# Performance work log

Measured on AMD Instinct MI355X. Metric: run time of the kernel, lower is better.

The kernel has to match this reference:

```python
import jax, jax.numpy as jnp
import numpy as np

N_MODEL = 1024
N_HEADS = 16
KV_HEADS = 4
HEAD_DIM = N_MODEL // N_HEADS          # 64
KV_MODEL = HEAD_DIM * KV_HEADS         # 256
GROUPS = N_HEADS // KV_HEADS           # 4
B, S = 4, 2048


def _rmsnorm(x):
    return x * jax.lax.rsqrt(jnp.mean(x * x, axis=-1, keepdims=True) + 1e-6)


def _act_quant(x):
    # 8-bit absmax per-token quantization (BitNet b1.58)
    scale = 127.0 / jnp.clip(jnp.max(jnp.abs(x), axis=-1, keepdims=True), 1e-5)
    return jnp.clip(jnp.round(x * scale), -128.0, 127.0) / scale


def _weight_quant(w):
    # ternary absmean quantization
    scale = 1.0 / jnp.clip(jnp.mean(jnp.abs(w)), 1e-5)
    return jnp.clip(jnp.round(w * scale), -1.0, 1.0) / scale


def bitlinear(x, w, b):
    xn = _rmsnorm(x)
    xq = xn + jax.lax.stop_gradient(_act_quant(xn) - xn)   # STE
    wq = w + jax.lax.stop_gradient(_weight_quant(w) - w)   # STE
    return jnp.einsum('...i,oi->...o', xq, wq) + b


def setup_inputs() -> dict:
    key = jax.random.key(0)
    ks = jax.random.split(key, 11)
    sq = 1.0 / np.sqrt(N_MODEL)
    sk = 1.0 / np.sqrt(KV_MODEL)
    return {
        'query': jax.random.normal(ks[0], (B, S, N_MODEL), jnp.float32),
        'key':   jax.random.normal(ks[1], (B, S, N_MODEL), jnp.float32),
        'value': jax.random.normal(ks[2], (B, S, N_MODEL), jnp.float32),
        'Wq': jax.random.normal(ks[3], (N_MODEL, N_MODEL), jnp.float32) * sq,
        'bq': jnp.zeros((N_MODEL,), jnp.float32),
        'Wk': jax.random.normal(ks[4], (KV_MODEL, N_MODEL), jnp.float32) * sq,
        'bk': jnp.zeros((KV_MODEL,), jnp.float32),
        'Wv': jax.random.normal(ks[5], (KV_MODEL, N_MODEL), jnp.float32) * sq,
        'bv': jnp.zeros((KV_MODEL,), jnp.float32),
        'Wo': jax.random.normal(ks[6], (N_MODEL, KV_MODEL), jnp.float32) * sk,
        'bo': jnp.zeros((N_MODEL,), jnp.float32),
    }


def reference(query, key, value, Wq, bq, Wk, bk, Wv, bv, Wo, bo):
    b = query.shape[0]
    Q = bitlinear(query, Wq, bq)   # [b, n, n_model]
    K = bitlinear(key,   Wk, bk)   # [b, s, kv_model]
    V = bitlinear(value, Wv, bv)   # [b, s, kv_model]

    # [b, h, n, d] layouts
    Q = Q.reshape(b, -1, N_HEADS, HEAD_DIM).transpose(0, 2, 1, 3)
    K = K.reshape(b, -1, KV_HEADS, HEAD_DIM).transpose(0, 2, 1, 3)
    V = V.reshape(b, -1, KV_HEADS, HEAD_DIM).transpose(0, 2, 1, 3)

    # group query heads: [b, g, kv_h, n, d]
    Qg = Q.reshape(b, KV_HEADS, GROUPS, -1, HEAD_DIM).transpose(0, 2, 1, 3, 4)
    # NOTE: faithful to the module, the einsum output has no 'g' axis,
    # so the grouped query heads are SUMMED over g.
    energy = jnp.einsum('bghnd,bhsd->bhns', Qg, K)  # [b, kv_h, n, s]

    scale = jnp.sqrt(jnp.float32(HEAD_DIM))
    attention = jax.nn.softmax(energy / scale, axis=-1)
    x = jnp.einsum('bhns,bhsd->bhnd', attention, V)  # [b, kv_h, n, d]
    x = x.transpose(0, 2, 1, 3).reshape(b, -1, KV_MODEL)
    x = bitlinear(x, Wo, bo)       # [b, n, n_model]
    return (x, attention)
```

## Files before the change

### kernel.cpp

```cpp
#include <hip/hip_runtime.h>
#include <stdint.h>

#define N_MODELC 1024
#define KV_MODELC 256
#define BATCH 4
#define SEQ 2048
#define NTOK (BATCH*SEQ)
#define NCHUNK 4
#define CHUNK (SEQ/NCHUNK)

typedef __attribute__((ext_vector_type(4))) float f32x4;
typedef __attribute__((ext_vector_type(4))) int   i32x4;
typedef __attribute__((ext_vector_type(8))) short s16x8;

__device__ __forceinline__ unsigned short f2bf(float f){
  unsigned u = __builtin_bit_cast(unsigned, f);
  u = (u + 0x7FFFu + ((u>>16)&1u)) >> 16;
  return (unsigned short)u;
}

__global__ __launch_bounds__(256) void k_actquant1024(
    const float* __restrict__ xq_in, const float* __restrict__ xk_in, const float* __restrict__ xv_in,
    int8_t* __restrict__ q8q, int8_t* __restrict__ q8k, int8_t* __restrict__ q8v,
    float* __restrict__ scq, float* __restrict__ sck, float* __restrict__ scv)
{
  int row = blockIdx.x, which = blockIdx.y, t = threadIdx.x;
  const float* x = (which==0)?xq_in:(which==1)?xk_in:xv_in;
  int8_t* q8 = (which==0)?q8q:(which==1)?q8k:q8v;
  float* sc = (which==0)?scq:(which==1)?sck:scv;
  const float* xr = x + (size_t)row*N_MODELC;
  float4 v = reinterpret_cast<const float4*>(xr)[t];
  float ss = v.x*v.x + v.y*v.y + v.z*v.z + v.w*v.w;
  float am = fmaxf(fmaxf(fabsf(v.x),fabsf(v.y)), fmaxf(fabsf(v.z),fabsf(v.w)));
  #pragma unroll
  for (int m=32;m;m>>=1){ ss += __shfl_xor(ss,m,64); am = fmaxf(am, __shfl_xor(am,m,64)); }
  __shared__ float red[8];
  int wid = t>>6;
  if ((t&63)==0){ red[wid]=ss; red[4+wid]=am; }
  __syncthreads();
  ss = red[0]+red[1]+red[2]+red[3];
  am = fmaxf(fmaxf(red[4],red[5]), fmaxf(red[6],red[7]));
  float rinv = rsqrtf(ss*(1.0f/N_MODELC) + 1e-6f);
  float clipv = fmaxf(am*rinv, 1e-5f);
  float qs = 127.0f/clipv;
  float fsc = rinv*qs;
  char4 o;
  o.x = (signed char)(int)fminf(127.f, fmaxf(-128.f, rintf(v.x*fsc)));
  o.y = (signed char)(int)fminf(127.f, fmaxf(-128.f, rintf(v.y*fsc)));
  o.z = (signed char)(int)fminf(127.f, fmaxf(-128.f, rintf(v.z*fsc)));
  o.w = (signed char)(int)fminf(127.f, fmaxf(-128.f, rintf(v.w*fsc)));
  reinterpret_cast<char4*>(q8 + (size_t)row*N_MODELC)[t] = o;
  if (t==0) sc[row] = clipv*(1.0f/127.0f);
}

__global__ __launch_bounds__(64) void k_actquant256(
    const float* __restrict__ X, int8_t* __restrict__ q8, float* __restrict__ sc)
{
  int row = blockIdx.x, l = threadIdx.x;
  float4 v = reinterpret_cast<const float4*>(X + (size_t)row*KV_MODELC)[l];
  float ss = v.x*v.x + v.y*v.y + v.z*v.z + v.w*v.w;
  float am = fmaxf(fmaxf(fabsf(v.x),fabsf(v.y)), fmaxf(fabsf(v.z),fabsf(v.w)));
  #pragma unroll
  for (int m=32;m;m>>=1){ ss += __shfl_xor(ss,m,64); am = fmaxf(am, __shfl_xor(am,m,64)); }
  float rinv = rsqrtf(ss*(1.0f/KV_MODELC) + 1e-6f);
  float clipv = fmaxf(am*rinv, 1e-5f);
  float qs = 127.0f/clipv;
  float fsc = rinv*qs;
  char4 o;
  o.x = (signed char)(int)fminf(127.f, fmaxf(-128.f, rintf(v.x*fsc)));
  o.y = (signed char)(int)fminf(127.f, fmaxf(-128.f, rintf(v.y*fsc)));
  o.z = (signed char)(int)fminf(127.f, fmaxf(-128.f, rintf(v.z*fsc)));
  o.w = (signed char)(int)fminf(127.f, fmaxf(-128.f, rintf(v.w*fsc)));
  reinterpret_cast<char4*>(q8 + (size_t)row*KV_MODELC)[l] = o;
  if (l==0) sc[row] = clipv*(1.0f/127.0f);
}

__global__ __launch_bounds__(256) void k_wabs_partial(
    const float* __restrict__ Wq, const float* __restrict__ Wk,
    const float* __restrict__ Wv, const float* __restrict__ Wo, float* __restrict__ partial)
{
  int mat = blockIdx.y;
  const float* w = (mat==0)?Wq:(mat==1)?Wk:(mat==2)?Wv:Wo;
  int n = (mat==0)?(N_MODELC*N_MODELC):(KV_MODELC*N_MODELC);
  float s = 0.f;
  for (int i = blockIdx.x*256 + threadIdx.x; i < n; i += 256*256) s += fabsf(w[i]);
  #pragma unroll
  for (int m=32;m;m>>=1) s += __shfl_xor(s,m,64);
  __shared__ float red[4];
  int wid = threadIdx.x>>6;
  if ((threadIdx.x&63)==0) red[wid]=s;
  __syncthreads();
  if (threadIdx.x==0) partial[mat*256 + blockIdx.x] = red[0]+red[1]+red[2]+red[3];
}

__global__ __launch_bounds__(256) void k_wfinal(const float* __restrict__ partial, float* __restrict__ wfac)
{
  int mat = blockIdx.x, t = threadIdx.x;
  float s = partial[mat*256 + t];
  #pragma unroll
  for (int m=32;m;m>>=1) s += __shfl_xor(s,m,64);
  __shared__ float red[4];
  int wid = t>>6;
  if ((t&63)==0) red[wid]=s;
  __syncthreads();
  if (t==0){
    float tot = red[0]+red[1]+red[2]+red[3];
    float n = (mat==0)?(float)(N_MODELC*N_MODELC):(float)(KV_MODELC*N_MODELC);
    wfac[mat] = fmaxf(tot/n, 1e-5f);
  }
}

__global__ __launch_bounds__(256) void k_tern(
    const float* __restrict__ Wq, const float* __restrict__ Wk,
    const float* __restrict__ Wv, const float* __restrict__ Wo,
    const float* __restrict__ wfac,
    int8_t* __restrict__ Wqs, int8_t* __restrict__ Wkt,
    int8_t* __restrict__ Wvt, int8_t* __restrict__ Wot)
{
  int mat = blockIdx.y;
  int idx = blockIdx.x*256 + threadIdx.x;
  if (mat==0){
    float s = 1.0f/wfac[0];
    int op = idx>>10, i = idx&1023;
    int kv = op>>6, d = op&63;
    int acc = 0;
    #pragma unroll
    for (int g=0; g<4; g++){
      float w = Wq[(size_t)(kv*256 + g*64 + d)*N_MODELC + i];
      float r = fminf(1.f, fmaxf(-1.f, rintf(w*s)));
      acc += (int)r;
    }
    Wqs[idx] = (int8_t)acc;
  } else {
    const float* w = (mat==1)?Wk:(mat==2)?Wv:Wo;
    int8_t* o = (mat==1)?Wkt:(mat==2)?Wvt:Wot;
    float s = 1.0f/wfac[mat];
    float r = fminf(1.f, fmaxf(-1.f, rintf(w[idx]*s)));
    o[idx] = (int8_t)r;
  }
}

template<int KDIM, int MODE>
__global__ __launch_bounds__(256) void k_gemm_i8(
    const int8_t* __restrict__ A, const int8_t* __restrict__ B,
    const float* __restrict__ rowscale, const float* __restrict__ wfac, int wfi,
    const float* __restrict__ bias, void* __restrict__ outp)
{
  int mb = blockIdx.x*64, nb = blockIdx.y*64;
  int w = threadIdx.x>>6, l = threadIdx.x&63, lr = l&15, lk = l>>4;
  const int8_t* Ap = A + (size_t)(mb + w*16 + lr)*KDIM + lk*16;
  const int8_t* Bp = B + (size_t)(nb + lr)*KDIM + lk*16;
  i32x4 acc[4];
  #pragma unroll
  for (int f=0; f<4; f++) acc[f] = i32x4{0,0,0,0};
  #pragma unroll 4
  for (int kk=0; kk<KDIM; kk+=64){
    i32x4 a = *reinterpret_cast<const i32x4*>(Ap + kk);
    #pragma unroll
    for (int f=0; f<4; f++){
      i32x4 b = *reinterpret_cast<const i32x4*>(Bp + (size_t)f*16*KDIM + kk);
      acc[f] = __builtin_amdgcn_mfma_i32_16x16x64_i8(a, b, acc[f], 0, 0, 0);
    }
  }
  float wf = wfac[wfi];
  #pragma unroll
  for (int f=0; f<4; f++){
    int col = nb + f*16 + lr;
    float bval;
    if constexpr (MODE==0){
      int kv = col>>6, d = col&63;
      const float* bb = bias + kv*256 + d;
      bval = bb[0]+bb[64]+bb[128]+bb[192];
    } else {
      bval = bias[col];
    }
    #pragma unroll
    for (int r=0; r<4; r++){
      int row = mb + w*16 + lk*4 + r;
      float val = (float)acc[f][r] * (rowscale[row]*wf) + bval;
      if constexpr (MODE==0){
        ((unsigned short*)outp)[(size_t)row*KV_MODELC + col] = f2bf(0.125f*val);
      } else if constexpr (MODE==1){
        ((unsigned short*)outp)[(size_t)row*KV_MODELC + col] = f2bf(val);
      } else if constexpr (MODE==2){
        int bi = row>>11, s = row&2047;
        ((unsigned short*)outp)[((size_t)(bi*256 + col))*SEQ + s] = f2bf(val);
      } else {
        ((float*)outp)[(size_t)row*N_MODELC + col] = val;
      }
    }
  }
}

__global__ __launch_bounds__(256) void k_attn1(
    const unsigned short* __restrict__ Qs, const unsigned short* __restrict__ Kb,
    float* __restrict__ mpart, float* __restrict__ lpart)
{
  int bkv = blockIdx.y, b = bkv>>2, kv = bkv&3;
  int c = blockIdx.z;
  int w = threadIdx.x>>6, l = threadIdx.x&63, lr = l&15, lk = l>>4;
  int rowt = blockIdx.x*64 + w*16;
  size_t tq = (size_t)(b*SEQ + rowt + lr)*KV_MODELC + kv*64 + lk*8;
  s16x8 qa0 = *reinterpret_cast<const s16x8*>(Qs + tq);
  s16x8 qa1 = *reinterpret_cast<const s16x8*>(Qs + tq + 32);
  const unsigned short* kbase = Kb + (size_t)b*SEQ*KV_MODELC + kv*64 + lk*8;
  float m[4], ll[4];
  #pragma unroll
  for (int r=0;r<4;r++){ m[r] = -INFINITY; ll[r] = 0.f; }
  for (int st=c*CHUNK; st<(c+1)*CHUNK; st+=16){
    const unsigned short* kp = kbase + (size_t)(st+lr)*KV_MODELC;
    s16x8 k0 = *reinterpret_cast<const s16x8*>(kp);
    s16x8 k1 = *reinterpret_cast<const s16x8*>(kp + 32);
    f32x4 acc = {0.f,0.f,0.f,0.f};
    acc = __builtin_amdgcn_mfma_f32_16x16x32_bf16(qa0, k0, acc, 0,0,0);
    acc = __builtin_amdgcn_mfma_f32_16x16x32_bf16(qa1, k1, acc, 0,0,0);
    #pragma unroll
    for (int r=0;r<4;r++){
      float e = acc[r];
      float mn = fmaxf(m[r], e);
      ll[r] = ll[r]*__expf(m[r]-mn) + __expf(e-mn);
      m[r] = mn;
    }
  }
  #pragma unroll
  for (int r=0;r<4;r++){
    #pragma unroll
    for (int mask=1; mask<16; mask<<=1){
      float om = __shfl_xor(m[r], mask, 64);
      float ol = __shfl_xor(ll[r], mask, 64);
      float mn = fmaxf(m[r], om);
      ll[r] = ll[r]*__expf(m[r]-mn) + ol*__expf(om-mn);
      m[r] = mn;
    }
  }
  if (lr==0){
    #pragma unroll
    for (int r=0;r<4;r++){
      size_t idx = ((size_t)(c*16 + bkv))*SEQ + rowt + lk*4 + r;
      mpart[idx] = m[r];
      lpart[idx] = ll[r];
    }
  }
}

__global__ __launch_bounds__(256) void k_attn2(
    const unsigned short* __restrict__ Qs, const unsigned short* __restrict__ Kb,
    const unsigned short* __restrict__ VT,
    const float* __restrict__ mpart, const float* __restrict__ lpart,
    float* __restrict__ attn, float* __restrict__ pvpart)
{
  __shared__ unsigned short plds[64][64];
  int bkv = blockIdx.y, b = bkv>>2, kv = bkv&3;
  int c = blockIdx.z;
  int w = threadIdx.x>>6, l = threadIdx.x&63, lr = l&15, lk = l>>4;
  int brow = blockIdx.x*64;
  int rowt = brow + w*16;
  size_t tq = (size_t)(b*SEQ + rowt + lr)*KV_MODELC + kv*64 + lk*8;
  s16x8 qa0 = *reinterpret_cast<const s16x8*>(Qs + tq);
  s16x8 qa1 = *reinterpret_cast<const s16x8*>(Qs + tq + 32);
  const unsigned short* kbase = Kb + (size_t)b*SEQ*KV_MODELC + kv*64 + lk*8;
  const unsigned short* vbase = VT + ((size_t)(b*256 + kv*64))*SEQ;

  float m[4], invl[4];
  #pragma unroll
  for (int r=0;r<4;r++){
    int row = rowt + lk*4 + r;
    float M = -INFINITY, L = 0.f;
    #pragma unroll
    for (int cc=0; cc<NCHUNK; cc++){
      size_t idx = ((size_t)(cc*16 + bkv))*SEQ + row;
      float mm = mpart[idx], lw = lpart[idx];
      float mn = fmaxf(M, mm);
      L = L*__expf(M-mn) + lw*__expf(mm-mn);
      M = mn;
    }
    m[r] = M; invl[r] = 1.0f/L;
  }

  float* arow = attn + (size_t)bkv*SEQ*SEQ + (size_t)brow*SEQ;
  f32x4 acco[4];
  #pragma unroll
  for (int dt=0; dt<4; dt++) acco[dt] = f32x4{0.f,0.f,0.f,0.f};
  int qw = w*16 + lk*4;
  int qr = w*16 + lr;
  int rsw = (qr&7)<<3;

  for (int st=c*CHUNK; st<(c+1)*CHUNK; st+=64){
    #pragma unroll
    for (int sub=0; sub<4; sub++){
      int s0 = st + sub*16;
      const unsigned short* kp = kbase + (size_t)(s0+lr)*KV_MODELC;
      s16x8 k0 = *reinterpret_cast<const s16x8*>(kp);
      s16x8 k1 = *reinterpret_cast<const s16x8*>(kp + 32);
      f32x4 acc = {0.f,0.f,0.f,0.f};
      acc = __builtin_amdgcn_mfma_f32_16x16x32_bf16(qa0, k0, acc, 0,0,0);
      acc = __builtin_amdgcn_mfma_f32_16x16x32_bf16(qa1, k1, acc, 0,0,0);
      int slocal = sub*16 + lr;
      #pragma unroll
      for (int r=0;r<4;r++){
        float p = __expf(acc[r]-m[r])*invl[r];
        arow[(size_t)(qw + r)*SEQ + s0 + lr] = p;
        int sw = (slocal & 7) | ((((slocal>>3) ^ ((qw+r)&7)))<<3);
        plds[qw + r][sw] = f2bf(p);
      }
    }
    s16x8 a0 = *reinterpret_cast<const s16x8*>(&plds[qr][(lk<<3) ^ rsw]);
    s16x8 a1 = *reinterpret_cast<const s16x8*>(&plds[qr][((4+lk)<<3) ^ rsw]);
    #pragma unroll
    for (int dt=0; dt<4; dt++){
      const unsigned short* vp = vbase + (size_t)(dt*16+lr)*SEQ + st + lk*8;
      s16x8 b0 = *reinterpret_cast<const s16x8*>(vp);
      s16x8 b1 = *reinterpret_cast<const s16x8*>(vp + 32);
      acco[dt] = __builtin_amdgcn_mfma_f32_16x16x32_bf16(a0, b0, acco[dt], 0,0,0);
      acco[dt] = __builtin_amdgcn_mfma_f32_16x16x32_bf16(a1, b1, acco[dt], 0,0,0);
    }
  }
  #pragma unroll
  for (int dt=0; dt<4; dt++){
    #pragma unroll
    for (int r=0; r<4; r++){
      int row = rowt + lk*4 + r;
      pvpart[(((size_t)(c*16 + bkv))*SEQ + row)*64 + dt*16 + lr] = acco[dt][r];
    }
  }
}

__global__ __launch_bounds__(256) void k_pvsum(
    const float* __restrict__ pvpart, float* __restrict__ X)
{
  size_t idx = (size_t)blockIdx.x*256 + threadIdx.x;
  int d = idx & 63;
  int row = (int)((idx>>6) & (SEQ-1));
  int bkv = (int)(idx >> 17);
  float s = 0.f;
  #pragma unroll
  for (int c=0; c<NCHUNK; c++)
    s += pvpart[(((size_t)(c*16 + bkv))*SEQ + row)*64 + d];
  int b = bkv>>2, kv = bkv&3;
  X[((size_t)(b*SEQ + row))*KV_MODELC + kv*64 + d] = s;
}

extern "C" void kernel_launch(void* const* d_in, const int* in_sizes, int n_in,
                              void* d_out, int out_size, void* d_ws, size_t ws_size,
                              hipStream_t stream)
{
  (void)in_sizes; (void)n_in; (void)out_size; (void)ws_size;
  const float* q  = (const float*)d_in[0];
  const float* k  = (const float*)d_in[1];
  const float* v  = (const float*)d_in[2];
  const float* Wq = (const float*)d_in[3];
  const float* bq = (const float*)d_in[4];
  const float* Wk = (const float*)d_in[5];
  const float* bk = (const float*)d_in[6];
  const float* Wv = (const float*)d_in[7];
  const float* bv = (const float*)d_in[8];
  const float* Wo = (const float*)d_in[9];
  const float* bo = (const float*)d_in[10];

  float* out_x = (float*)d_out;
  float* out_attn = out_x + (size_t)NTOK*N_MODELC;

  char* ws = (char*)d_ws;
  size_t off = 0;
  auto alloc = [&](size_t bytes)->void*{
    void* p = ws + off; off += (bytes + 255) & ~(size_t)255; return p;
  };
  int8_t* q8q = (int8_t*)alloc((size_t)NTOK*N_MODELC);
  int8_t* q8k = (int8_t*)alloc((size_t)NTOK*N_MODELC);
  int8_t* q8v = (int8_t*)alloc((size_t)NTOK*N_MODELC);
  int8_t* q8x = (int8_t*)alloc((size_t)NTOK*KV_MODELC);
  float* scq = (float*)alloc(NTOK*4);
  float* sck = (float*)alloc(NTOK*4);
  float* scv = (float*)alloc(NTOK*4);
  float* scx = (float*)alloc(NTOK*4);
  float* partial = (float*)alloc(4*256*4);
  float* wfac = (float*)alloc(256);
  int8_t* Wqs = (int8_t*)alloc(256*1024);
  int8_t* Wkt = (int8_t*)alloc(256*1024);
  int8_t* Wvt = (int8_t*)alloc(256*1024);
  int8_t* Wot = (int8_t*)alloc(1024*256);
  unsigned short* Qs = (unsigned short*)alloc((size_t)NTOK*KV_MODELC*2);
  unsigned short* Kb = (unsigned short*)alloc((size_t)NTOK*KV_MODELC*2);
  unsigned short* VT = (unsigned short*)alloc((size_t)NTOK*KV_MODELC*2);
  float* X = (float*)alloc((size_t)NTOK*KV_MODELC*4);
  float* mpart = (float*)alloc((size_t)NCHUNK*16*SEQ*4);
  float* lpart = (float*)alloc((size_t)NCHUNK*16*SEQ*4);
  float* pvpart = (float*)alloc((size_t)NCHUNK*16*SEQ*64*4);

  hipLaunchKernelGGL(k_actquant1024, dim3(NTOK,3), dim3(256), 0, stream,
                     q,k,v, q8q,q8k,q8v, scq,sck,scv);
  hipLaunchKernelGGL(k_wabs_partial, dim3(256,4), dim3(256), 0, stream, Wq,Wk,Wv,Wo, partial);
  hipLaunchKernelGGL(k_wfinal, dim3(4), dim3(256), 0, stream, partial, wfac);
  hipLaunchKernelGGL(k_tern, dim3(1024,4), dim3(256), 0, stream,
                     Wq,Wk,Wv,Wo, wfac, Wqs,Wkt,Wvt,Wot);
  hipLaunchKernelGGL((k_gemm_i8<1024,0>), dim3(128,4), dim3(256), 0, stream,
                     q8q, Wqs, scq, wfac, 0, bq, (void*)Qs);
  hipLaunchKernelGGL((k_gemm_i8<1024,1>), dim3(128,4), dim3(256), 0, stream,
                     q8k, Wkt, sck, wfac, 1, bk, (void*)Kb);
  hipLaunchKernelGGL((k_gemm_i8<1024,2>), dim3(128,4), dim3(256), 0, stream,
                     q8v, Wvt, scv, wfac, 2, bv, (void*)VT);
  hipLaunchKernelGGL(k_attn1, dim3(32,16,NCHUNK), dim3(256), 0, stream,
                     Qs, Kb, mpart, lpart);
  hipLaunchKernelGGL(k_attn2, dim3(32,16,NCHUNK), dim3(256), 0, stream,
                     Qs, Kb, VT, mpart, lpart, out_attn, pvpart);
  hipLaunchKernelGGL(k_pvsum, dim3(16*SEQ*64/256), dim3(256), 0, stream,
                     pvpart, X);
  hipLaunchKernelGGL(k_actquant256, dim3(NTOK), dim3(64), 0, stream, X, q8x, scx);
  hipLaunchKernelGGL((k_gemm_i8<256,3>), dim3(128,16), dim3(256), 0, stream,
                     q8x, Wot, scx, wfac, 3, bo, (void*)out_x);
}
```

Before: 351.1 us.

## Split-K QKV GEMMs, coalesce attention-prob stores, and vectorize partial-PV layout

The 1024-K int8 GEMMs now run 512 threads, with two K-halves reduced through LDS. The V-transpose output is staged in LDS so it can be written with 16-byte stores. The attention-probability output is written as coalesced float4 rows read back from the bf16 LDS tile, replacing scattered scalar stores. Partial PV accumulators are stored in native MFMA fragment order as f32x4, and k_pvsum transposes them through LDS for vectorized writes. The main intent is cutting uncoalesced global writes, especially the large attention matrix. The risk is that the stored attention probabilities are now bf16-rounded.

```diff
diff --git a/kernel.cpp b/kernel.cpp
--- a/kernel.cpp
+++ b/kernel.cpp
@@ -12,11 +12,15 @@
 typedef __attribute__((ext_vector_type(4))) float f32x4;
 typedef __attribute__((ext_vector_type(4))) int   i32x4;
 typedef __attribute__((ext_vector_type(8))) short s16x8;
+typedef __attribute__((ext_vector_type(4))) short s16x4;
 
 __device__ __forceinline__ unsigned short f2bf(float f){
   unsigned u = __builtin_bit_cast(unsigned, f);
   u = (u + 0x7FFFu + ((u>>16)&1u)) >> 16;
   return (unsigned short)u;
+}
+__device__ __forceinline__ float bf2f(unsigned short b){
+  return __builtin_bit_cast(float, ((unsigned)b)<<16);
 }
 
 __global__ __launch_bounds__(256) void k_actquant1024(
@@ -140,12 +144,81 @@
   }
 }
 
-template<int KDIM, int MODE>
-__global__ __launch_bounds__(256) void k_gemm_i8(
+template<int MODE>
+__global__ __launch_bounds__(512) void k_gemm_i8_1024(
     const int8_t* __restrict__ A, const int8_t* __restrict__ B,
     const float* __restrict__ rowscale, const float* __restrict__ wfac, int wfi,
-    const float* __restrict__ bias, void* __restrict__ outp)
-{
+    const float* __restrict__ bias, unsigned short* __restrict__ outp)
+{
+  __shared__ i32x4 redk[4][4][64];
+  __shared__ unsigned short tlds[(MODE==2)?64:1][72];
+  const int KDIM = 1024;
+  int mb = blockIdx.x*64, nb = blockIdx.y*64;
+  int w = threadIdx.x>>6, l = threadIdx.x&63, lr = l&15, lk = l>>4;
+  int rw = w&3, kh = w>>2;
+  const int8_t* Ap = A + (size_t)(mb + rw*16 + lr)*KDIM + kh*512 + lk*16;
+  const int8_t* Bp = B + (size_t)(nb + lr)*KDIM + kh*512 + lk*16;
+  i32x4 acc[4];
+  #pragma unroll
+  for (int f=0; f<4; f++) acc[f] = i32x4{0,0,0,0};
+  #pragma unroll 4
+  for (int kk=0; kk<512; kk+=64){
+    i32x4 a = *reinterpret_cast<const i32x4*>(Ap + kk);
+    #pragma unroll
+    for (int f=0; f<4; f++){
+      i32x4 b = *reinterpret_cast<const i32x4*>(Bp + (size_t)f*16*KDIM + kk);
+      acc[f] = __builtin_amdgcn_mfma_i32_16x16x64_i8(a, b, acc[f], 0, 0, 0);
+    }
+  }
+  if (kh==1){
+    #pragma unroll
+    for (int f=0; f<4; f++) redk[rw][f][l] = acc[f];
+  }
+  __syncthreads();
+  if (kh==0){
+    float wf = wfac[wfi];
+    #pragma unroll
+    for (int f=0; f<4; f++){
+      acc[f] += redk[rw][f][l];
+      int col = nb + f*16 + lr;
+      float bval;
+      if constexpr (MODE==0){
+        int kv = col>>6, d = col&63;
+        const float* bb = bias + kv*256 + d;
+        bval = bb[0]+bb[64]+bb[128]+bb[192];
+      } else {
+        bval = bias[col];
+      }
+      #pragma unroll
+      for (int r=0; r<4; r++){
+        int row = mb + rw*16 + lk*4 + r;
+        float val = (float)acc[f][r] * (rowscale[row]*wf) + bval;
+        if constexpr (MODE==0){
+          outp[(size_t)row*KV_MODELC + col] = f2bf(0.125f*val);
+        } else if constexpr (MODE==1){
+          outp[(size_t)row*KV_MODELC + col] = f2bf(val);
+        } else {
+          tlds[f*16+lr][rw*16 + lk*4 + r] = f2bf(val);
+        }
+      }
+    }
+  }
+  if constexpr (MODE==2){
+    __syncthreads();
+    int u = threadIdx.x;
+    int col = u>>3, part = u&7;
+    int b = mb>>11, s0 = mb&2047;
+    s16x8 vv = *reinterpret_cast<const s16x8*>(&tlds[col][part*8]);
+    *reinterpret_cast<s16x8*>(&outp[((size_t)(b*256 + nb + col))*SEQ + s0 + part*8]) = vv;
+  }
+}
+
+__global__ __launch_bounds__(256) void k_gemm_o(
+    const int8_t* __restrict__ A, const int8_t* __restrict__ B,
+    const float* __restrict__ rowscale, const float* __restrict__ wfac,
+    const float* __restrict__ bias, float* __restrict__ outp)
+{
+  const int KDIM = 256;
   int mb = blockIdx.x*64, nb = blockIdx.y*64;
   int w = threadIdx.x>>6, l = threadIdx.x&63, lr = l&15, lk = l>>4;
   const int8_t* Ap = A + (size_t)(mb + w*16 + lr)*KDIM + lk*16;
@@ -153,7 +226,7 @@
   i32x4 acc[4];
   #pragma unroll
   for (int f=0; f<4; f++) acc[f] = i32x4{0,0,0,0};
-  #pragma unroll 4
+  #pragma unroll
   for (int kk=0; kk<KDIM; kk+=64){
     i32x4 a = *reinterpret_cast<const i32x4*>(Ap + kk);
     #pragma unroll
@@ -162,32 +235,15 @@
       acc[f] = __builtin_amdgcn_mfma_i32_16x16x64_i8(a, b, acc[f], 0, 0, 0);
     }
   }
-  float wf = wfac[wfi];
+  float wf = wfac[3];
   #pragma unroll
   for (int f=0; f<4; f++){
     int col = nb + f*16 + lr;
-    float bval;
-    if constexpr (MODE==0){
-      int kv = col>>6, d = col&63;
-      const float* bb = bias + kv*256 + d;
-      bval = bb[0]+bb[64]+bb[128]+bb[192];
-    } else {
-      bval = bias[col];
-    }
+    float bval = bias[col];
     #pragma unroll
     for (int r=0; r<4; r++){
       int row = mb + w*16 + lk*4 + r;
-      float val = (float)acc[f][r] * (rowscale[row]*wf) + bval;
-      if constexpr (MODE==0){
-        ((unsigned short*)outp)[(size_t)row*KV_MODELC + col] = f2bf(0.125f*val);
-      } else if constexpr (MODE==1){
-        ((unsigned short*)outp)[(size_t)row*KV_MODELC + col] = f2bf(val);
-      } else if constexpr (MODE==2){
-        int bi = row>>11, s = row&2047;
-        ((unsigned short*)outp)[((size_t)(bi*256 + col))*SEQ + s] = f2bf(val);
-      } else {
-        ((float*)outp)[(size_t)row*N_MODELC + col] = val;
-      }
+      outp[(size_t)row*N_MODELC + col] = (float)acc[f][r]*(rowscale[row]*wf) + bval;
     }
   }
 }
@@ -299,7 +355,6 @@
       #pragma unroll
       for (int r=0;r<4;r++){
         float p = __expf(acc[r]-m[r])*invl[r];
-        arow[(size_t)(qw + r)*SEQ + s0 + lr] = p;
         int sw = (slocal & 7) | ((((slocal>>3) ^ ((qw+r)&7)))<<3);
         plds[qw + r][sw] = f2bf(p);
       }
@@ -314,13 +369,27 @@
       acco[dt] = __builtin_amdgcn_mfma_f32_16x16x32_bf16(a0, b0, acco[dt], 0,0,0);
       acco[dt] = __builtin_amdgcn_mfma_f32_16x16x32_bf16(a1, b1, acco[dt], 0,0,0);
     }
-  }
-  #pragma unroll
-  for (int dt=0; dt<4; dt++){
-    #pragma unroll
-    for (int r=0; r<4; r++){
-      int row = rowt + lk*4 + r;
-      pvpart[(((size_t)(c*16 + bkv))*SEQ + row)*64 + dt*16 + lr] = acco[dt][r];
+    #pragma unroll
+    for (int j=0; j<4; j++){
+      int row = w*16 + j*4 + (l>>4);
+      int sseg = l & 15;
+      int chunk = sseg >> 1, half = sseg & 1;
+      int off = ((chunk ^ (row&7)) << 3) + (half<<2);
+      s16x4 pb = *reinterpret_cast<const s16x4*>(&plds[row][off]);
+      float4 pv4;
+      pv4.x = bf2f((unsigned short)pb[0]);
+      pv4.y = bf2f((unsigned short)pb[1]);
+      pv4.z = bf2f((unsigned short)pb[2]);
+      pv4.w = bf2f((unsigned short)pb[3]);
+      *reinterpret_cast<float4*>(&arow[(size_t)row*SEQ + st + sseg*4]) = pv4;
+    }
+  }
+  {
+    int T = (bkv*32 + blockIdx.x)*4 + w;
+    float* base = pvpart + ((size_t)c*2048 + T)*1024;
+    #pragma unroll
+    for (int dt=0; dt<4; dt++){
+      *reinterpret_cast<f32x4*>(base + (dt*64 + l)*4) = acco[dt];
     }
   }
 }
@@ -328,16 +397,27 @@
 __global__ __launch_bounds__(256) void k_pvsum(
     const float* __restrict__ pvpart, float* __restrict__ X)
 {
-  size_t idx = (size_t)blockIdx.x*256 + threadIdx.x;
-  int d = idx & 63;
-  int row = (int)((idx>>6) & (SEQ-1));
-  int bkv = (int)(idx >> 17);
-  float s = 0.f;
-  #pragma unroll
-  for (int c=0; c<NCHUNK; c++)
-    s += pvpart[(((size_t)(c*16 + bkv))*SEQ + row)*64 + d];
+  __shared__ float xls[16][65];
+  int T = blockIdx.x;
+  int w = T&3, qblk = (T>>2)&31, bkv = T>>7;
   int b = bkv>>2, kv = bkv&3;
-  X[((size_t)(b*SEQ + row))*KV_MODELC + kv*64 + d] = s;
+  int t = threadIdx.x;
+  int dt = t>>6, l = t&63;
+  f32x4 s = {0.f,0.f,0.f,0.f};
+  #pragma unroll
+  for (int c=0; c<NCHUNK; c++){
+    f32x4 v = *reinterpret_cast<const f32x4*>(pvpart + ((size_t)c*2048 + T)*1024 + t*4);
+    s += v;
+  }
+  int lk = l>>4, lr = l&15;
+  #pragma unroll
+  for (int r=0; r<4; r++) xls[lk*4+r][dt*16+lr] = s[r];
+  __syncthreads();
+  int row = t>>4, col4 = (t&15)*4;
+  float4 o;
+  o.x = xls[row][col4]; o.y = xls[row][col4+1];
+  o.z = xls[row][col4+2]; o.w = xls[row][col4+3];
+  *reinterpret_cast<float4*>(&X[((size_t)(b*SEQ + qblk*64 + w*16 + row))*KV_MODELC + kv*64 + col4]) = o;
 }
 
 extern "C" void kernel_launch(void* const* d_in, const int* in_sizes, int n_in,
@@ -385,7 +465,7 @@
   float* X = (float*)alloc((size_t)NTOK*KV_MODELC*4);
   float* mpart = (float*)alloc((size_t)NCHUNK*16*SEQ*4);
   float* lpart = (float*)alloc((size_t)NCHUNK*16*SEQ*4);
-  float* pvpart = (float*)alloc((size_t)NCHUNK*16*SEQ*64*4);
+  float* pvpart = (float*)alloc((size_t)NCHUNK*2048*1024*4);
 
   hipLaunchKernelGGL(k_actquant1024, dim3(NTOK,3), dim3(256), 0, stream,
                      q,k,v, q8q,q8k,q8v, scq,sck,scv);
@@ -393,19 +473,18 @@
   hipLaunchKernelGGL(k_wfinal, dim3(4), dim3(256), 0, stream, partial, wfac);
   hipLaunchKernelGGL(k_tern, dim3(1024,4), dim3(256), 0, stream,
                      Wq,Wk,Wv,Wo, wfac, Wqs,Wkt,Wvt,Wot);
-  hipLaunchKernelGGL((k_gemm_i8<1024,0>), dim3(128,4), dim3(256), 0, stream,
-                     q8q, Wqs, scq, wfac, 0, bq, (void*)Qs);
-  hipLaunchKernelGGL((k_gemm_i8<1024,1>), dim3(128,4), dim3(256), 0, stream,
-                     q8k, Wkt, sck, wfac, 1, bk, (void*)Kb);
-  hipLaunchKernelGGL((k_gemm_i8<1024,2>), dim3(128,4), dim3(256), 0, stream,
-                     q8v, Wvt, scv, wfac, 2, bv, (void*)VT);
+  hipLaunchKernelGGL((k_gemm_i8_1024<0>), dim3(128,4), dim3(512), 0, stream,
+                     q8q, Wqs, scq, wfac, 0, bq, Qs);
+  hipLaunchKernelGGL((k_gemm_i8_1024<1>), dim3(128,4), dim3(512), 0, stream,
+                     q8k, Wkt, sck, wfac, 1, bk, Kb);
+  hipLaunchKernelGGL((k_gemm_i8_1024<2>), dim3(128,4), dim3(512), 0, stream,
+                     q8v, Wvt, scv, wfac, 2, bv, VT);
   hipLaunchKernelGGL(k_attn1, dim3(32,16,NCHUNK), dim3(256), 0, stream,
                      Qs, Kb, mpart, lpart);
   hipLaunchKernelGGL(k_attn2, dim3(32,16,NCHUNK), dim3(256), 0, stream,
                      Qs, Kb, VT, mpart, lpart, out_attn, pvpart);
-  hipLaunchKernelGGL(k_pvsum, dim3(16*SEQ*64/256), dim3(256), 0, stream,
-                     pvpart, X);
+  hipLaunchKernelGGL(k_pvsum, dim3(2048), dim3(256), 0, stream, pvpart, X);
   hipLaunchKernelGGL(k_actquant256, dim3(NTOK), dim3(64), 0, stream, X, q8x, scx);
-  hipLaunchKernelGGL((k_gemm_i8<256,3>), dim3(128,16), dim3(256), 0, stream,
-                     q8x, Wot, scx, wfac, 3, bo, (void*)out_x);
-}
+  hipLaunchKernelGGL(k_gemm_o, dim3(128,16), dim3(256), 0, stream,
+                     q8x, Wot, scx, wfac, bo, out_x);
+}
```

Result: faster. 336.3 us (-4.2%).
